# Kernel tuning notes

Measured on AMD Instinct MI355X. Metric: run time of the kernel, lower is better.

Reference implementation:

```python
import jax, jax.numpy as jnp
import numpy as np

IMG = 128; P = 16; ND = IMG // P; N = ND * ND  # 64 patches
INF = 3 * P * P      # 768 flattened patch features
ATT = 768; HID = 3072; OUT = 768; B = 64
EPS = 1e-5


def setup_inputs() -> dict:
    key = jax.random.key(0)
    ks = jax.random.split(key, 24)
    w = lambda k, shape: jax.random.normal(k, shape, jnp.float32) * 0.02
    return {
        "x": jax.random.normal(ks[0], (B, 3, IMG, IMG), jnp.float32),
        # per-patch q/k/v projections: [n, in, out] weights, [n, out] biases
        "Wq": w(ks[1], (N, INF, ATT)), "bq": w(ks[2], (N, ATT)),
        "Wk": w(ks[3], (N, INF, ATT)), "bk": w(ks[4], (N, ATT)),
        "Wv": w(ks[5], (N, INF, ATT)), "bv": w(ks[6], (N, ATT)),
        "ln_g": jnp.ones((ATT,), jnp.float32), "ln_b": jnp.zeros((ATT,), jnp.float32),
        "p1_w": w(ks[7], (INF, ATT)), "p1_b": w(ks[8], (ATT,)),
        "w0": w(ks[9], (ATT, HID)),  "b0": w(ks[10], (HID,)),
        "w1": w(ks[11], (HID, HID)), "b1": w(ks[12], (HID,)),
        "w2": w(ks[13], (HID, HID)), "b2": w(ks[14], (HID,)),
        "w3": w(ks[15], (HID, HID)), "b3": w(ks[16], (HID,)),
        "w4": w(ks[17], (HID, OUT)), "b4": w(ks[18], (OUT,)),
        "p2_w": w(ks[19], (ATT, OUT)), "p2_b": w(ks[20], (OUT,)),
    }


def _forward(x, Wq, bq, Wk, bk, Wv, bv, ln_g, ln_b, p1_w, p1_b,
             w0, b0, w1, b1, w2, b2, w3, b3, w4, b4, p2_w, p2_b):
    b_ = x.shape[0]
    # patch split (row-major over (i,j) blocks) then flatten channel*patch dims
    flat = x.reshape(b_, 3, ND, P, ND, P).transpose(0, 2, 4, 1, 3, 5).reshape(b_, N, INF)
    # per-patch projections, attention taken ACROSS the batch dim (as in source)
    q = jnp.einsum('bnf,nfd->bnd', flat, Wq) + bq
    k = jnp.einsum('bnf,nfd->bnd', flat, Wk) + bk
    v = jnp.einsum('bnf,nfd->bnd', flat, Wv) + bv
    scores = jnp.einsum('bnd,cnd->nbc', q, k) / jnp.sqrt(jnp.float32(ATT))  # [n,B,B]
    attn = jnp.einsum('nbc,cnd->bnd', jax.nn.softmax(scores, axis=-1), v)  # [B,n,ATT]
    # LayerNorm(att_features)
    mu = attn.mean(-1, keepdims=True)
    var = ((attn - mu) ** 2).mean(-1, keepdims=True)
    ln = (attn - mu) / jnp.sqrt(var + EPS) * ln_g + ln_b
    att = ln + flat @ p1_w + p1_b
    # linear stack (no nonlinearity in the source)
    h = att @ w0 + b0
    h = h @ w1 + b1
    h = h @ w2 + b2
    h = h @ w3 + b3
    h = h @ w4 + b4
    proj = h + att @ p2_w + p2_b
    return jax.nn.softmax(proj, axis=2)


def reference(x, Wq, bq, Wk, bk, Wv, bv, ln_g, ln_b, p1_w, p1_b,
              w0, b0, w1, b1, w2, b2, w3, b3, w4, b4, p2_w, p2_b):
    return _forward(x, Wq, bq, Wk, bk, Wv, bv, ln_g, ln_b, p1_w, p1_b,
                    w0, b0, w1, b1, w2, b2, w3, b3, w4, b4, p2_w, p2_b)
```

## Files before the change

kernel.cpp:

```cpp
#include <hip/hip_runtime.h>
#include <hip/hip_bf16.h>

using bf16 = __bf16;
using bf16x8 = __bf16 __attribute__((ext_vector_type(8)));
using f32x4 = float __attribute__((ext_vector_type(4)));

static constexpr long ROWEL = 64L * 768;

__device__ __forceinline__ void async16(void* lds, const void* g)
{
    __builtin_amdgcn_global_load_lds((const __attribute__((address_space(1))) void*)g,
                                     (__attribute__((address_space(3))) void*)lds, 16, 0, 0);
}

__global__ __launch_bounds__(256) void k_patchify(const float* __restrict__ x, bf16* __restrict__ flat)
{
    const int n = blockIdx.x;
    const int b = blockIdx.y;
    const int i_ = n >> 3, j_ = n & 7;
    for (int it = 0; it < 3; ++it) {
        int f = threadIdx.x + it * 256;
        int c = f >> 8, rem = f & 255, pi = rem >> 4, pj = rem & 15;
        float v = x[(((long)(b * 3 + c)) << 14) + ((i_ * 16 + pi) << 7) + (j_ * 16 + pj)];
        flat[(long)b * ROWEL + n * 768 + f] = (bf16)v;
    }
}

__global__ __launch_bounds__(256) void k_cvt_t(const float* __restrict__ W, bf16* __restrict__ Wt,
                                               int Kd, int Nd)
{
    __shared__ bf16 T[64 * 66];
    const int k0 = blockIdx.x * 64, n0 = blockIdx.y * 64;
    const int tid = threadIdx.x;
    const int kr = tid >> 4, nc = (tid & 15) * 4;
#pragma unroll
    for (int i = 0; i < 4; ++i) {
        f32x4 v = *(const f32x4*)(W + (long)(k0 + kr + i * 16) * Nd + n0 + nc);
#pragma unroll
        for (int e = 0; e < 4; ++e)
            T[(kr + i * 16) * 66 + nc + e] = (bf16)v[e];
    }
    __syncthreads();
    const int nr = tid >> 3, ks = (tid & 7) * 8;
#pragma unroll
    for (int it = 0; it < 2; ++it) {
        int n = nr + it * 32;
        bf16x8 o;
#pragma unroll
        for (int j = 0; j < 8; ++j) o[j] = T[(ks + j) * 66 + n];
        *(bf16x8*)(Wt + (long)(n0 + n) * Kd + k0 + ks) = o;
    }
}

__global__ __launch_bounds__(256) void k_cast(const float* __restrict__ W, bf16* __restrict__ o, long nelem)
{
    long i = ((long)blockIdx.x * 256 + threadIdx.x) * 8;
    if (i >= nelem) return;
    f32x4 a = *(const f32x4*)(W + i);
    f32x4 b = *(const f32x4*)(W + i + 4);
    bf16x8 v;
#pragma unroll
    for (int e = 0; e < 4; ++e) { v[e] = (bf16)a[e]; v[4 + e] = (bf16)b[e]; }
    *(bf16x8*)(o + i) = v;
}

template<int BM, int BN>
__global__ __launch_bounds__(256) void k_gemm_bt(
    const bf16* __restrict__ A, long lda,
    const bf16* __restrict__ Bt, long ldb,
    int K,
    const float* __restrict__ bias,
    const float* __restrict__ addm,
    bf16* __restrict__ Cb, float* __restrict__ Cf, long ldc)
{
    constexpr int WM = BM / 2, WN = BN / 2, FM = WM / 16, FN = WN / 16;
    __shared__ bf16 As[BM * 32];
    __shared__ bf16 Bs[BN * 32];
    const int tid = threadIdx.x, lane = tid & 63, wave = tid >> 6;
    const int wm = wave >> 1, wn = wave & 1;
    const long m0 = (long)blockIdx.x * BM, n0 = (long)blockIdx.y * BN;

    f32x4 acc[FM][FN];
#pragma unroll
    for (int i = 0; i < FM; ++i)
#pragma unroll
        for (int j = 0; j < FN; ++j) acc[i][j] = (f32x4){0.f, 0.f, 0.f, 0.f};

    const int nk = K >> 5;
    for (int kt = 0; kt < nk; ++kt) {
        const long kb = (long)kt * 32;
#pragma unroll
        for (int i = 0; i < BM / 64; ++i) {
            const int idx = tid + i * 256;
            const int r = idx >> 2, seg = idx & 3;
            async16(&As[(i * 256 + wave * 64) * 8], A + (m0 + r) * lda + kb + seg * 8);
        }
#pragma unroll
        for (int i = 0; i < BN / 64; ++i) {
            const int idx = tid + i * 256;
            const int r = idx >> 2, seg = idx & 3;
            async16(&Bs[(i * 256 + wave * 64) * 8], Bt + (n0 + r) * ldb + kb + seg * 8);
        }
        __syncthreads();
        bf16x8 af[FM], bfr[FN];
#pragma unroll
        for (int i = 0; i < FM; ++i)
            af[i] = *(const bf16x8*)&As[(wm * WM + i * 16 + (lane & 15)) * 32 + (lane >> 4) * 8];
#pragma unroll
        for (int j = 0; j < FN; ++j)
            bfr[j] = *(const bf16x8*)&Bs[(wn * WN + j * 16 + (lane & 15)) * 32 + (lane >> 4) * 8];
#pragma unroll
        for (int i = 0; i < FM; ++i)
#pragma unroll
            for (int j = 0; j < FN; ++j)
                acc[i][j] = __builtin_amdgcn_mfma_f32_16x16x32_bf16(af[i], bfr[j], acc[i][j], 0, 0, 0);
        __syncthreads();
    }

#pragma unroll
    for (int j = 0; j < FN; ++j) {
        const long col = n0 + wn * WN + j * 16 + (lane & 15);
        const float bb = bias ? bias[col] : 0.f;
#pragma unroll
        for (int i = 0; i < FM; ++i) {
#pragma unroll
            for (int r = 0; r < 4; ++r) {
                const long row = m0 + wm * WM + i * 16 + (lane >> 4) * 4 + r;
                const long idx = row * ldc + col;
                float v = acc[i][j][r] + bb;
                if (addm) v += addm[idx];
                if (Cb) Cb[idx] = (bf16)v;
                if (Cf) Cf[idx] = v;
            }
        }
    }
}

__global__ __launch_bounds__(256) void k_qkv(
    const bf16* __restrict__ flat, const float* __restrict__ W, const float* __restrict__ bias,
    bf16* __restrict__ out)
{
    __shared__ bf16 As[64 * 32];
    __shared__ float Bs[32 * 64];
    const int tid = threadIdx.x, lane = tid & 63, wave = tid >> 6;
    const int wm = wave >> 1, wn = wave & 1;
    const int n0 = blockIdx.x * 64;
    const int z = blockIdx.y;
    const float* Wz = W + (long)z * 589824;

    f32x4 acc[2][2];
#pragma unroll
    for (int i = 0; i < 2; ++i)
#pragma unroll
        for (int j = 0; j < 2; ++j) acc[i][j] = (f32x4){0.f, 0.f, 0.f, 0.f};

    for (int kt = 0; kt < 24; ++kt) {
        const int kb = kt * 32;
        {
            const int r = tid >> 2, seg = tid & 3;
            async16(&As[wave * 512], flat + (long)r * ROWEL + z * 768 + kb + seg * 8);
        }
#pragma unroll
        for (int i = 0; i < 2; ++i) {
            const int g = i * 4 + wave;
            const int kk = kb + g * 4 + (lane >> 4);
            const int nn = (lane & 15) * 4;
            async16(&Bs[g * 256], Wz + (long)kk * 768 + n0 + nn);
        }
        __syncthreads();
        bf16x8 af[2], bfr[2];
#pragma unroll
        for (int i = 0; i < 2; ++i)
            af[i] = *(const bf16x8*)&As[(wm * 32 + i * 16 + (lane & 15)) * 32 + (lane >> 4) * 8];
#pragma unroll
        for (int j = 0; j < 2; ++j) {
            const int n = wn * 32 + j * 16 + (lane & 15);
            const int kf = (lane >> 4) * 8;
            bf16x8 b;
#pragma unroll
            for (int e = 0; e < 8; ++e) b[e] = (bf16)Bs[(kf + e) * 64 + n];
            bfr[j] = b;
        }
#pragma unroll
        for (int i = 0; i < 2; ++i)
#pragma unroll
            for (int j = 0; j < 2; ++j)
                acc[i][j] = __builtin_amdgcn_mfma_f32_16x16x32_bf16(af[i], bfr[j], acc[i][j], 0, 0, 0);
        __syncthreads();
    }

#pragma unroll
    for (int j = 0; j < 2; ++j) {
        const int col = n0 + wn * 32 + j * 16 + (lane & 15);
        const float bb = bias[z * 768 + col];
#pragma unroll
        for (int i = 0; i < 2; ++i) {
#pragma unroll
            for (int r = 0; r < 4; ++r) {
                const int row = wm * 32 + i * 16 + (lane >> 4) * 4 + r;
                out[(long)row * ROWEL + z * 768 + col] = (bf16)(acc[i][j][r] + bb);
            }
        }
    }
}

__global__ __launch_bounds__(256) void k_vm(
    const float* __restrict__ vin, const float* __restrict__ W,
    int K, int N, float* __restrict__ outP)
{
    __shared__ float red[4][64];
    const int tid = threadIdx.x;
    const int nl = tid & 63, kq = tid >> 6;
    const int n = blockIdx.x * 64 + nl;
    const int kc = blockIdx.y;
    const int kchunk = K / 8, kslice = kchunk / 4;
    const int k0 = kc * kchunk + kq * kslice;
    float acc = 0.f;
#pragma unroll 8
    for (int k = k0; k < k0 + kslice; ++k)
        acc += vin[k] * W[(long)k * N + n];
    red[kq][nl] = acc;
    __syncthreads();
    if (kq == 0)
        outP[(long)kc * N + n] = red[0][nl] + red[1][nl] + red[2][nl] + red[3][nl];
}

__global__ __launch_bounds__(256) void k_vred(
    const float* __restrict__ P, const float* __restrict__ b1, const float* __restrict__ b2,
    int N, float* __restrict__ out)
{
    const int n = blockIdx.x * 256 + threadIdx.x;
    if (n >= N) return;
    float s = b1[n] + (b2 ? b2[n] : 0.f);
#pragma unroll
    for (int j = 0; j < 8; ++j) s += P[(long)j * N + n];
    out[n] = s;
}

__global__ __launch_bounds__(256) void k_madd(const float* __restrict__ MTf, const float* __restrict__ p2w,
                                              bf16* __restrict__ Mt)
{
    const int n = blockIdx.x;
    for (int k = threadIdx.x; k < 768; k += 256)
        Mt[n * 768 + k] = (bf16)(MTf[n * 768 + k] + p2w[(long)k * 768 + n]);
}

__global__ __launch_bounds__(256) void k_attn(
    const bf16* __restrict__ q, const bf16* __restrict__ k, const bf16* __restrict__ v,
    float* __restrict__ attn)
{
    const int n = blockIdx.x;
    __shared__ bf16 QT[64 * 72];
    __shared__ bf16 KT[64 * 72];
    __shared__ float S[64 * 66];
    __shared__ bf16 P[64 * 72];
    __shared__ bf16 VT[128 * 72];

    const int tid = threadIdx.x, lane = tid & 63, wave = tid >> 6;
    const int wm = wave >> 1, wn = wave & 1;

    f32x4 accs[2][2];
#pragma unroll
    for (int i = 0; i < 2; ++i)
#pragma unroll
        for (int j = 0; j < 2; ++j) accs[i][j] = (f32x4){0.f, 0.f, 0.f, 0.f};

    for (int kt = 0; kt < 12; ++kt) {
#pragma unroll
        for (int i = 0; i < 2; ++i) {
            int cid = tid + i * 256;
            int r = cid >> 3, seg = cid & 7;
            *(bf16x8*)&QT[r * 72 + seg * 8] = *(const bf16x8*)(q + (long)r * ROWEL + n * 768 + kt * 64 + seg * 8);
            *(bf16x8*)&KT[r * 72 + seg * 8] = *(const bf16x8*)(k + (long)r * ROWEL + n * 768 + kt * 64 + seg * 8);
        }
        __syncthreads();
#pragma unroll
        for (int ks = 0; ks < 2; ++ks) {
            bf16x8 qa[2], kb[2];
#pragma unroll
            for (int i = 0; i < 2; ++i)
                qa[i] = *(const bf16x8*)&QT[(wm * 32 + i * 16 + (lane & 15)) * 72 + ks * 32 + (lane >> 4) * 8];
#pragma unroll
            for (int j = 0; j < 2; ++j)
                kb[j] = *(const bf16x8*)&KT[(wn * 32 + j * 16 + (lane & 15)) * 72 + ks * 32 + (lane >> 4) * 8];
#pragma unroll
            for (int i = 0; i < 2; ++i)
#pragma unroll
                for (int j = 0; j < 2; ++j)
                    accs[i][j] = __builtin_amdgcn_mfma_f32_16x16x32_bf16(qa[i], kb[j], accs[i][j], 0, 0, 0);
        }
        __syncthreads();
    }
    const float sc = 0.03608439182435161f;
#pragma unroll
    for (int i = 0; i < 2; ++i)
#pragma unroll
        for (int j = 0; j < 2; ++j)
#pragma unroll
            for (int r = 0; r < 4; ++r)
                S[(wm * 32 + i * 16 + (lane >> 4) * 4 + r) * 66 + wn * 32 + j * 16 + (lane & 15)] = accs[i][j][r] * sc;
    __syncthreads();

    {
        int r = tid >> 2, l4 = tid & 3;
        float m = -1e30f;
        for (int c = l4; c < 64; c += 4) m = fmaxf(m, S[r * 66 + c]);
        m = fmaxf(m, __shfl_xor(m, 1));
        m = fmaxf(m, __shfl_xor(m, 2));
        float s = 0.f;
        for (int c = l4; c < 64; c += 4) { float e = __expf(S[r * 66 + c] - m); S[r * 66 + c] = e; s += e; }
        s += __shfl_xor(s, 1);
        s += __shfl_xor(s, 2);
        float inv = 1.f / s;
        for (int c = l4; c < 64; c += 4) P[r * 72 + c] = (bf16)(S[r * 66 + c] * inv);
    }
    __syncthreads();

    for (int dc = 0; dc < 6; ++dc) {
#pragma unroll
        for (int i = 0; i < 4; ++i) {
            int cid = tid + i * 256;
            int c = cid >> 4, seg = cid & 15;
            bf16x8 vv = *(const bf16x8*)(v + (long)c * ROWEL + n * 768 + dc * 128 + seg * 8);
#pragma unroll
            for (int e = 0; e < 8; ++e)
                VT[(seg * 8 + e) * 72 + c] = vv[e];
        }
        __syncthreads();
        f32x4 acco[2][4];
#pragma unroll
        for (int i = 0; i < 2; ++i)
#pragma unroll
            for (int j = 0; j < 4; ++j) acco[i][j] = (f32x4){0.f, 0.f, 0.f, 0.f};
#pragma unroll
        for (int ks = 0; ks < 2; ++ks) {
            bf16x8 pa[2], vb[4];
#pragma unroll
            for (int i = 0; i < 2; ++i)
                pa[i] = *(const bf16x8*)&P[(wm * 32 + i * 16 + (lane & 15)) * 72 + ks * 32 + (lane >> 4) * 8];
#pragma unroll
            for (int j = 0; j < 4; ++j)
                vb[j] = *(const bf16x8*)&VT[(wn * 64 + j * 16 + (lane & 15)) * 72 + ks * 32 + (lane >> 4) * 8];
#pragma unroll
            for (int i = 0; i < 2; ++i)
#pragma unroll
                for (int j = 0; j < 4; ++j)
                    acco[i][j] = __builtin_amdgcn_mfma_f32_16x16x32_bf16(pa[i], vb[j], acco[i][j], 0, 0, 0);
        }
#pragma unroll
        for (int i = 0; i < 2; ++i)
#pragma unroll
            for (int j = 0; j < 4; ++j)
#pragma unroll
                for (int r = 0; r < 4; ++r) {
                    long b = wm * 32 + i * 16 + (lane >> 4) * 4 + r;
                    int d = dc * 128 + wn * 64 + j * 16 + (lane & 15);
                    attn[b * ROWEL + n * 768 + d] = acco[i][j][r];
                }
        __syncthreads();
    }
}

__global__ __launch_bounds__(256) void k_ln(float* __restrict__ a,
                                            const float* __restrict__ g, const float* __restrict__ bb)
{
    const long row = blockIdx.x * 4 + (threadIdx.x >> 6);
    const int lane = threadIdx.x & 63;
    float* p = a + row * 768;
    f32x4 xv[3];
    float s = 0.f;
#pragma unroll
    for (int c = 0; c < 3; ++c) {
        xv[c] = *(const f32x4*)(p + c * 256 + lane * 4);
        s += xv[c][0] + xv[c][1] + xv[c][2] + xv[c][3];
    }
#pragma unroll
    for (int o = 1; o < 64; o <<= 1) s += __shfl_xor(s, o);
    const float mu = s * (1.f / 768.f);
    float vs = 0.f;
#pragma unroll
    for (int c = 0; c < 3; ++c)
#pragma unroll
        for (int e = 0; e < 4; ++e) { float d = xv[c][e] - mu; vs += d * d; }
#pragma unroll
    for (int o = 1; o < 64; o <<= 1) vs += __shfl_xor(vs, o);
    const float rstd = rsqrtf(vs * (1.f / 768.f) + 1e-5f);
#pragma unroll
    for (int c = 0; c < 3; ++c)
#pragma unroll
        for (int e = 0; e < 4; ++e) {
            int col = c * 256 + lane * 4 + e;
            p[col] = (xv[c][e] - mu) * rstd * g[col] + bb[col];
        }
}

__global__ __launch_bounds__(256) void k_softmax(float* __restrict__ o)
{
    const long row = blockIdx.x * 4 + (threadIdx.x >> 6);
    const int lane = threadIdx.x & 63;
    float* p = o + row * 768;
    f32x4 xv[3];
    float m = -1e30f;
#pragma unroll
    for (int c = 0; c < 3; ++c) {
        xv[c] = *(const f32x4*)(p + c * 256 + lane * 4);
        m = fmaxf(m, fmaxf(fmaxf(xv[c][0], xv[c][1]), fmaxf(xv[c][2], xv[c][3])));
    }
#pragma unroll
    for (int o2 = 1; o2 < 64; o2 <<= 1) m = fmaxf(m, __shfl_xor(m, o2));
    float s = 0.f;
#pragma unroll
    for (int c = 0; c < 3; ++c)
#pragma unroll
        for (int e = 0; e < 4; ++e) { float ev = __expf(xv[c][e] - m); xv[c][e] = ev; s += ev; }
#pragma unroll
    for (int o2 = 1; o2 < 64; o2 <<= 1) s += __shfl_xor(s, o2);
    const float inv = 1.f / s;
#pragma unroll
    for (int c = 0; c < 3; ++c)
        *(f32x4*)(p + c * 256 + lane * 4) = xv[c] * inv;
}

extern "C" void kernel_launch(void* const* d_in, const int* in_sizes, int n_in,
                              void* d_out, int out_size, void* d_ws, size_t ws_size,
                              hipStream_t stream)
{
    const float* x   = (const float*)d_in[0];
    const float* Wq  = (const float*)d_in[1];
    const float* bq  = (const float*)d_in[2];
    const float* Wk  = (const float*)d_in[3];
    const float* bk  = (const float*)d_in[4];
    const float* Wv  = (const float*)d_in[5];
    const float* bv  = (const float*)d_in[6];
    const float* lng = (const float*)d_in[7];
    const float* lnb = (const float*)d_in[8];
    const float* p1w = (const float*)d_in[9];
    const float* p1b = (const float*)d_in[10];
    const float* w0  = (const float*)d_in[11];
    const float* b0  = (const float*)d_in[12];
    const float* w1  = (const float*)d_in[13];
    const float* b1  = (const float*)d_in[14];
    const float* w2  = (const float*)d_in[15];
    const float* b2  = (const float*)d_in[16];
    const float* w3  = (const float*)d_in[17];
    const float* b3  = (const float*)d_in[18];
    const float* w4  = (const float*)d_in[19];
    const float* b4  = (const float*)d_in[20];
    const float* p2w = (const float*)d_in[21];
    const float* p2b = (const float*)d_in[22];
    float* out = (float*)d_out;

    char* wsbase = (char*)d_ws;
    size_t off = 0;
    auto alloc = [&](size_t bytes) { char* p = wsbase + off; off += (bytes + 255) & ~(size_t)255; return p; };
    bf16*  flat = (bf16*)alloc(4096L * 768 * 2);
    bf16*  qb   = (bf16*)alloc(4096L * 768 * 2);
    bf16*  kb   = (bf16*)alloc(4096L * 768 * 2);
    bf16*  vb2  = (bf16*)alloc(4096L * 768 * 2);
    float* attn = (float*)alloc(4096L * 768 * 4);
    bf16*  att  = (bf16*)alloc(4096L * 768 * 2);
    bf16*  p1t  = (bf16*)alloc(768L * 768 * 2);
    bf16*  w0c  = (bf16*)alloc(768L * 3072 * 2);
    bf16*  w1c  = (bf16*)alloc(3072L * 3072 * 2);
    bf16*  w2c  = (bf16*)alloc(3072L * 3072 * 2);
    bf16*  w3c  = (bf16*)alloc(3072L * 3072 * 2);
    bf16*  w4t  = (bf16*)alloc(768L * 3072 * 2);
    bf16*  M1   = (bf16*)alloc(768L * 3072 * 2);
    bf16*  M2   = (bf16*)alloc(768L * 3072 * 2);
    float* MTf  = (float*)alloc(768L * 768 * 4);
    bf16*  Mt   = (bf16*)alloc(768L * 768 * 2);
    float* vP   = (float*)alloc(8L * 3072 * 4);
    float* c1   = (float*)alloc(3072 * 4);
    float* c2   = (float*)alloc(3072 * 4);
    float* c3   = (float*)alloc(3072 * 4);
    float* c4   = (float*)alloc(768 * 4);
    if (off > ws_size) return;

    k_patchify<<<dim3(64, 64), 256, 0, stream>>>(x, flat);
    k_qkv<<<dim3(12, 64), 256, 0, stream>>>(flat, Wq, bq, qb);
    k_qkv<<<dim3(12, 64), 256, 0, stream>>>(flat, Wk, bk, kb);
    k_qkv<<<dim3(12, 64), 256, 0, stream>>>(flat, Wv, bv, vb2);
    k_attn<<<64, 256, 0, stream>>>(qb, kb, vb2, attn);
    k_ln<<<1024, 256, 0, stream>>>(attn, lng, lnb);
    k_cvt_t<<<dim3(12, 12), 256, 0, stream>>>(p1w, p1t, 768, 768);
    k_gemm_bt<64, 128><<<dim3(64, 6), 256, 0, stream>>>(flat, 768, p1t, 768, 768, p1b, attn, att, nullptr, 768);

    k_cvt_t<<<dim3(48, 12), 256, 0, stream>>>(w4, w4t, 3072, 768);
    k_cast<<<4608, 256, 0, stream>>>(w1, w1c, 3072L * 3072);
    k_cast<<<4608, 256, 0, stream>>>(w2, w2c, 3072L * 3072);
    k_cast<<<4608, 256, 0, stream>>>(w3, w3c, 3072L * 3072);
    k_cast<<<1152, 256, 0, stream>>>(w0, w0c, 768L * 3072);

    k_gemm_bt<64, 128><<<dim3(12, 24), 256, 0, stream>>>(w4t, 3072, w3c, 3072, 3072, nullptr, nullptr, M1, nullptr, 3072);
    k_gemm_bt<64, 128><<<dim3(12, 24), 256, 0, stream>>>(M1, 3072, w2c, 3072, 3072, nullptr, nullptr, M2, nullptr, 3072);
    k_gemm_bt<64, 128><<<dim3(12, 24), 256, 0, stream>>>(M2, 3072, w1c, 3072, 3072, nullptr, nullptr, M1, nullptr, 3072);
    k_gemm_bt<64, 64><<<dim3(12, 12), 256, 0, stream>>>(M1, 3072, w0c, 3072, 3072, nullptr, nullptr, nullptr, MTf, 768);
    k_madd<<<768, 256, 0, stream>>>(MTf, p2w, Mt);

    k_vm<<<dim3(48, 8), 256, 0, stream>>>(b0, w1, 3072, 3072, vP);
    k_vred<<<12, 256, 0, stream>>>(vP, b1, nullptr, 3072, c1);
    k_vm<<<dim3(48, 8), 256, 0, stream>>>(c1, w2, 3072, 3072, vP);
    k_vred<<<12, 256, 0, stream>>>(vP, b2, nullptr, 3072, c2);
    k_vm<<<dim3(48, 8), 256, 0, stream>>>(c2, w3, 3072, 3072, vP);
    k_vred<<<12, 256, 0, stream>>>(vP, b3, nullptr, 3072, c3);
    k_vm<<<dim3(12, 8), 256, 0, stream>>>(c3, w4, 3072, 768, vP);
    k_vred<<<3, 256, 0, stream>>>(vP, b4, p2b, 768, c4);

    k_gemm_bt<64, 128><<<dim3(64, 6), 256, 0, stream>>>(att, 768, Mt, 768, 768, c4, nullptr, nullptr, out, 768);
    k_softmax<<<1024, 256, 0, stream>>>(out);
}
```

Baseline: 509.9 us.

## Double-buffer GEMM staging, batch launches, fuse bias-chain reductions and transpose-add epilogue

Adds double-buffered LDS staging to the generic GEMM and the per-patch QKV kernel so the next K tile loads while the current one computes. Merges the QKV, cast and transpose launches into single grids using blockIdx.z or y, folds the p2_w transposed add into the last weight-chain GEMM epilogue (removing k_madd and the fp32 intermediate), and fuses the bias-chain partial reductions into the next vector-matrix kernel reading bf16 weights. The weight-chain GEMMs switch to 64x64 tiles for more blocks. Reading bf16 weights in the bias chain lowers precision slightly, and the transposed add in the epilogue reads with a strided pattern.

Result: slower. 606.5 us (+19.0%).

```diff
diff --git a/kernel.cpp b/kernel.cpp
--- a/kernel.cpp
+++ b/kernel.cpp
@@ -26,9 +26,15 @@
     }
 }
 
-__global__ __launch_bounds__(256) void k_cvt_t(const float* __restrict__ W, bf16* __restrict__ Wt,
-                                               int Kd, int Nd)
-{
+__global__ __launch_bounds__(256) void k_cvt_t2(
+    const float* __restrict__ W0, bf16* __restrict__ T0,
+    const float* __restrict__ W1, bf16* __restrict__ T1)
+{
+    const int z = blockIdx.z;
+    const float* W = z ? W1 : W0;
+    bf16* Wt = z ? T1 : T0;
+    const int Kd = z ? 768 : 3072, Nd = 768;
+    if (z && blockIdx.x >= 12) return;
     __shared__ bf16 T[64 * 66];
     const int k0 = blockIdx.x * 64, n0 = blockIdx.y * 64;
     const int tid = threadIdx.x;
@@ -52,8 +58,16 @@
     }
 }
 
-__global__ __launch_bounds__(256) void k_cast(const float* __restrict__ W, bf16* __restrict__ o, long nelem)
-{
+__global__ __launch_bounds__(256) void k_cast4(
+    const float* __restrict__ s0, bf16* __restrict__ d0,
+    const float* __restrict__ s1, bf16* __restrict__ d1,
+    const float* __restrict__ s2, bf16* __restrict__ d2,
+    const float* __restrict__ s3, bf16* __restrict__ d3)
+{
+    const int z = blockIdx.y;
+    const float* W = z == 0 ? s0 : z == 1 ? s1 : z == 2 ? s2 : s3;
+    bf16* o = z == 0 ? d0 : z == 1 ? d1 : z == 2 ? d2 : d3;
+    const long nelem = z == 0 ? 768L * 3072 : 3072L * 3072;
     long i = ((long)blockIdx.x * 256 + threadIdx.x) * 8;
     if (i >= nelem) return;
     f32x4 a = *(const f32x4*)(W + i);
@@ -71,11 +85,12 @@
     int K,
     const float* __restrict__ bias,
     const float* __restrict__ addm,
+    const float* __restrict__ addt, long atld,
     bf16* __restrict__ Cb, float* __restrict__ Cf, long ldc)
 {
     constexpr int WM = BM / 2, WN = BN / 2, FM = WM / 16, FN = WN / 16;
-    __shared__ bf16 As[BM * 32];
-    __shared__ bf16 Bs[BN * 32];
+    __shared__ bf16 As[2][BM * 32];
+    __shared__ bf16 Bs[2][BN * 32];
     const int tid = threadIdx.x, lane = tid & 63, wave = tid >> 6;
     const int wm = wave >> 1, wn = wave & 1;
     const long m0 = (long)blockIdx.x * BM, n0 = (long)blockIdx.y * BN;
@@ -87,34 +102,42 @@
         for (int j = 0; j < FN; ++j) acc[i][j] = (f32x4){0.f, 0.f, 0.f, 0.f};
 
     const int nk = K >> 5;
+
+    auto stage = [&](int buf, int kt) {
+        const long kb = (long)kt * 32;
+#pragma unroll
+        for (int i = 0; i < BM / 64; ++i) {
+            const int c = i * 256 + tid;
+            const int r = c >> 2, seg = c & 3;
+            async16(&As[buf][(i * 256 + wave * 64) * 8], A + (m0 + r) * lda + kb + seg * 8);
+        }
+#pragma unroll
+        for (int i = 0; i < BN / 64; ++i) {
+            const int c = i * 256 + tid;
+            const int r = c >> 2, seg = c & 3;
+            async16(&Bs[buf][(i * 256 + wave * 64) * 8], Bt + (n0 + r) * ldb + kb + seg * 8);
+        }
+    };
+
+    stage(0, 0);
+    __syncthreads();
+    int cur = 0;
     for (int kt = 0; kt < nk; ++kt) {
-        const long kb = (long)kt * 32;
-#pragma unroll
-        for (int i = 0; i < BM / 64; ++i) {
-            const int idx = tid + i * 256;
-            const int r = idx >> 2, seg = idx & 3;
-            async16(&As[(i * 256 + wave * 64) * 8], A + (m0 + r) * lda + kb + seg * 8);
-        }
-#pragma unroll
-        for (int i = 0; i < BN / 64; ++i) {
-            const int idx = tid + i * 256;
-            const int r = idx >> 2, seg = idx & 3;
-            async16(&Bs[(i * 256 + wave * 64) * 8], Bt + (n0 + r) * ldb + kb + seg * 8);
-        }
-        __syncthreads();
+        if (kt + 1 < nk) stage(cur ^ 1, kt + 1);
         bf16x8 af[FM], bfr[FN];
 #pragma unroll
         for (int i = 0; i < FM; ++i)
-            af[i] = *(const bf16x8*)&As[(wm * WM + i * 16 + (lane & 15)) * 32 + (lane >> 4) * 8];
+            af[i] = *(const bf16x8*)&As[cur][(wm * WM + i * 16 + (lane & 15)) * 32 + (lane >> 4) * 8];
 #pragma unroll
         for (int j = 0; j < FN; ++j)
-            bfr[j] = *(const bf16x8*)&Bs[(wn * WN + j * 16 + (lane & 15)) * 32 + (lane >> 4) * 8];
+            bfr[j] = *(const bf16x8*)&Bs[cur][(wn * WN + j * 16 + (lane & 15)) * 32 + (lane >> 4) * 8];
 #pragma unroll
         for (int i = 0; i < FM; ++i)
 #pragma unroll
             for (int j = 0; j < FN; ++j)
                 acc[i][j] = __builtin_amdgcn_mfma_f32_16x16x32_bf16(af[i], bfr[j], acc[i][j], 0, 0, 0);
         __syncthreads();
+        cur ^= 1;
     }
 
 #pragma unroll
@@ -129,6 +152,7 @@
                 const long idx = row * ldc + col;
                 float v = acc[i][j][r] + bb;
                 if (addm) v += addm[idx];
+                if (addt) v += addt[col * atld + row];
                 if (Cb) Cb[idx] = (bf16)v;
                 if (Cf) Cf[idx] = v;
             }
@@ -137,11 +161,18 @@
 }
 
 __global__ __launch_bounds__(256) void k_qkv(
-    const bf16* __restrict__ flat, const float* __restrict__ W, const float* __restrict__ bias,
-    bf16* __restrict__ out)
-{
-    __shared__ bf16 As[64 * 32];
-    __shared__ float Bs[32 * 64];
+    const bf16* __restrict__ flat,
+    const float* __restrict__ Wq, const float* __restrict__ Wk, const float* __restrict__ Wv,
+    const float* __restrict__ bq, const float* __restrict__ bk, const float* __restrict__ bv,
+    bf16* __restrict__ qo, bf16* __restrict__ ko, bf16* __restrict__ vo)
+{
+    const int zz = blockIdx.z;
+    const float* W = zz == 0 ? Wq : zz == 1 ? Wk : Wv;
+    const float* bias = zz == 0 ? bq : zz == 1 ? bk : bv;
+    bf16* out = zz == 0 ? qo : zz == 1 ? ko : vo;
+
+    __shared__ bf16 As[2][64 * 32];
+    __shared__ float Bs[2][32 * 64];
     const int tid = threadIdx.x, lane = tid & 63, wave = tid >> 6;
     const int wm = wave >> 1, wn = wave & 1;
     const int n0 = blockIdx.x * 64;
@@ -154,31 +185,36 @@
 #pragma unroll
         for (int j = 0; j < 2; ++j) acc[i][j] = (f32x4){0.f, 0.f, 0.f, 0.f};
 
-    for (int kt = 0; kt < 24; ++kt) {
+    auto stage = [&](int buf, int kt) {
         const int kb = kt * 32;
         {
             const int r = tid >> 2, seg = tid & 3;
-            async16(&As[wave * 512], flat + (long)r * ROWEL + z * 768 + kb + seg * 8);
+            async16(&As[buf][wave * 512], flat + (long)r * ROWEL + z * 768 + kb + seg * 8);
         }
 #pragma unroll
         for (int i = 0; i < 2; ++i) {
-            const int g = i * 4 + wave;
-            const int kk = kb + g * 4 + (lane >> 4);
-            const int nn = (lane & 15) * 4;
-            async16(&Bs[g * 256], Wz + (long)kk * 768 + n0 + nn);
-        }
-        __syncthreads();
+            const int c = i * 256 + tid;
+            const int kl = c >> 4, nn = (c & 15) * 4;
+            async16(&Bs[buf][(i * 256 + wave * 64) * 4], Wz + (long)(kb + kl) * 768 + n0 + nn);
+        }
+    };
+
+    stage(0, 0);
+    __syncthreads();
+    int cur = 0;
+    for (int kt = 0; kt < 24; ++kt) {
+        if (kt + 1 < 24) stage(cur ^ 1, kt + 1);
         bf16x8 af[2], bfr[2];
 #pragma unroll
         for (int i = 0; i < 2; ++i)
-            af[i] = *(const bf16x8*)&As[(wm * 32 + i * 16 + (lane & 15)) * 32 + (lane >> 4) * 8];
+            af[i] = *(const bf16x8*)&As[cur][(wm * 32 + i * 16 + (lane & 15)) * 32 + (lane >> 4) * 8];
 #pragma unroll
         for (int j = 0; j < 2; ++j) {
             const int n = wn * 32 + j * 16 + (lane & 15);
             const int kf = (lane >> 4) * 8;
             bf16x8 b;
 #pragma unroll
-            for (int e = 0; e < 8; ++e) b[e] = (bf16)Bs[(kf + e) * 64 + n];
+            for (int e = 0; e < 8; ++e) b[e] = (bf16)Bs[cur][(kf + e) * 64 + n];
             bfr[j] = b;
         }
 #pragma unroll
@@ -187,6 +223,7 @@
             for (int j = 0; j < 2; ++j)
                 acc[i][j] = __builtin_amdgcn_mfma_f32_16x16x32_bf16(af[i], bfr[j], acc[i][j], 0, 0, 0);
         __syncthreads();
+        cur ^= 1;
     }
 
 #pragma unroll
@@ -204,9 +241,10 @@
     }
 }
 
-__global__ __launch_bounds__(256) void k_vm(
-    const float* __restrict__ vin, const float* __restrict__ W,
-    int K, int N, float* __restrict__ outP)
+template<typename TW>
+__global__ __launch_bounds__(256) void k_vm2(
+    const float* __restrict__ Pin, const float* __restrict__ bin, const TW* __restrict__ W,
+    int K, int N, float* __restrict__ Pout)
 {
     __shared__ float red[4][64];
     const int tid = threadIdx.x;
@@ -216,13 +254,19 @@
     const int kchunk = K / 8, kslice = kchunk / 4;
     const int k0 = kc * kchunk + kq * kslice;
     float acc = 0.f;
-#pragma unroll 8
-    for (int k = k0; k < k0 + kslice; ++k)
-        acc += vin[k] * W[(long)k * N + n];
+#pragma unroll 4
+    for (int k = k0; k < k0 + kslice; ++k) {
+        float vk = bin[k];
+        if (Pin) {
+#pragma unroll
+            for (int j = 0; j < 8; ++j) vk += Pin[(long)j * K + k];
+        }
+        acc += vk * (float)W[(long)k * N + n];
+    }
     red[kq][nl] = acc;
     __syncthreads();
     if (kq == 0)
-        outP[(long)kc * N + n] = red[0][nl] + red[1][nl] + red[2][nl] + red[3][nl];
+        Pout[(long)kc * N + n] = red[0][nl] + red[1][nl] + red[2][nl] + red[3][nl];
 }
 
 __global__ __launch_bounds__(256) void k_vred(
@@ -235,14 +279,6 @@
 #pragma unroll
     for (int j = 0; j < 8; ++j) s += P[(long)j * N + n];
     out[n] = s;
-}
-
-__global__ __launch_bounds__(256) void k_madd(const float* __restrict__ MTf, const float* __restrict__ p2w,
-                                              bf16* __restrict__ Mt)
-{
-    const int n = blockIdx.x;
-    for (int k = threadIdx.x; k < 768; k += 256)
-        Mt[n * 768 + k] = (bf16)(MTf[n * 768 + k] + p2w[(long)k * 768 + n]);
 }
 
 __global__ __launch_bounds__(256) void k_attn(
@@ -460,52 +496,41 @@
     float* attn = (float*)alloc(4096L * 768 * 4);
     bf16*  att  = (bf16*)alloc(4096L * 768 * 2);
     bf16*  p1t  = (bf16*)alloc(768L * 768 * 2);
+    bf16*  w4t  = (bf16*)alloc(768L * 3072 * 2);
     bf16*  w0c  = (bf16*)alloc(768L * 3072 * 2);
     bf16*  w1c  = (bf16*)alloc(3072L * 3072 * 2);
     bf16*  w2c  = (bf16*)alloc(3072L * 3072 * 2);
     bf16*  w3c  = (bf16*)alloc(3072L * 3072 * 2);
-    bf16*  w4t  = (bf16*)alloc(768L * 3072 * 2);
     bf16*  M1   = (bf16*)alloc(768L * 3072 * 2);
     bf16*  M2   = (bf16*)alloc(768L * 3072 * 2);
-    float* MTf  = (float*)alloc(768L * 768 * 4);
+    bf16*  M3   = (bf16*)alloc(768L * 3072 * 2);
     bf16*  Mt   = (bf16*)alloc(768L * 768 * 2);
-    float* vP   = (float*)alloc(8L * 3072 * 4);
-    float* c1   = (float*)alloc(3072 * 4);
-    float* c2   = (float*)alloc(3072 * 4);
-    float* c3   = (float*)alloc(3072 * 4);
+    float* vPa  = (float*)alloc(8L * 3072 * 4);
+    float* vPb  = (float*)alloc(8L * 3072 * 4);
     float* c4   = (float*)alloc(768 * 4);
     if (off > ws_size) return;
 
     k_patchify<<<dim3(64, 64), 256, 0, stream>>>(x, flat);
-    k_qkv<<<dim3(12, 64), 256, 0, stream>>>(flat, Wq, bq, qb);
-    k_qkv<<<dim3(12, 64), 256, 0, stream>>>(flat, Wk, bk, kb);
-    k_qkv<<<dim3(12, 64), 256, 0, stream>>>(flat, Wv, bv, vb2);
+    k_cast4<<<dim3(4608, 4), 256, 0, stream>>>(w0, w0c, w1, w1c, w2, w2c, w3, w3c);
+    k_cvt_t2<<<dim3(48, 12, 2), 256, 0, stream>>>(w4, w4t, p1w, p1t);
+
+    k_qkv<<<dim3(12, 64, 3), 256, 0, stream>>>(flat, Wq, Wk, Wv, bq, bk, bv, qb, kb, vb2);
+
     k_attn<<<64, 256, 0, stream>>>(qb, kb, vb2, attn);
     k_ln<<<1024, 256, 0, stream>>>(attn, lng, lnb);
-    k_cvt_t<<<dim3(12, 12), 256, 0, stream>>>(p1w, p1t, 768, 768);
-    k_gemm_bt<64, 128><<<dim3(64, 6), 256, 0, stream>>>(flat, 768, p1t, 768, 768, p1b, attn, att, nullptr, 768);
-
-    k_cvt_t<<<dim3(48, 12), 256, 0, stream>>>(w4, w4t, 3072, 768);
-    k_cast<<<4608, 256, 0, stream>>>(w1, w1c, 3072L * 3072);
-    k_cast<<<4608, 256, 0, stream>>>(w2, w2c, 3072L * 3072);
-    k_cast<<<4608, 256, 0, stream>>>(w3, w3c, 3072L * 3072);
-    k_cast<<<1152, 256, 0, stream>>>(w0, w0c, 768L * 3072);
-
-    k_gemm_bt<64, 128><<<dim3(12, 24), 256, 0, stream>>>(w4t, 3072, w3c, 3072, 3072, nullptr, nullptr, M1, nullptr, 3072);
-    k_gemm_bt<64, 128><<<dim3(12, 24), 256, 0, stream>>>(M1, 3072, w2c, 3072, 3072, nullptr, nullptr, M2, nullptr, 3072);
-    k_gemm_bt<64, 128><<<dim3(12, 24), 256, 0, stream>>>(M2, 3072, w1c, 3072, 3072, nullptr, nullptr, M1, nullptr, 3072);
-    k_gemm_bt<64, 64><<<dim3(12, 12), 256, 0, stream>>>(M1, 3072, w0c, 3072, 3072, nullptr, nullptr, nullptr, MTf, 768);
-    k_madd<<<768, 256, 0, stream>>>(MTf, p2w, Mt);
-
-    k_vm<<<dim3(48, 8), 256, 0, stream>>>(b0, w1, 3072, 3072, vP);
-    k_vred<<<12, 256, 0, stream>>>(vP, b1, nullptr, 3072, c1);
-    k_vm<<<dim3(48, 8), 256, 0, stream>>>(c1, w2, 3072, 3072, vP);
-    k_vred<<<12, 256, 0, stream>>>(vP, b2, nullptr, 3072, c2);
-    k_vm<<<dim3(48, 8), 256, 0, stream>>>(c2, w3, 3072, 3072, vP);
-    k_vred<<<12, 256, 0, stream>>>(vP, b3, nullptr, 3072, c3);
-    k_vm<<<dim3(12, 8), 256, 0, stream>>>(c3, w4, 3072, 768, vP);
-    k_vred<<<3, 256, 0, stream>>>(vP, b4, p2b, 768, c4);
-
-    k_gemm_bt<64, 128><<<dim3(64, 6), 256, 0, stream>>>(att, 768, Mt, 768, 768, c4, nullptr, nullptr, out, 768);
+    k_gemm_bt<64, 128><<<dim3(64, 6), 256, 0, stream>>>(flat, 768, p1t, 768, 768, p1b, attn, nullptr, 0, att, nullptr, 768);
+
+    k_gemm_bt<64, 64><<<dim3(12, 48), 256, 0, stream>>>(w4t, 3072, w3c, 3072, 3072, nullptr, nullptr, nullptr, 0, M1, nullptr, 3072);
+    k_gemm_bt<64, 64><<<dim3(12, 48), 256, 0, stream>>>(M1, 3072, w2c, 3072, 3072, nullptr, nullptr, nullptr, 0, M2, nullptr, 3072);
+    k_gemm_bt<64, 64><<<dim3(12, 48), 256, 0, stream>>>(M2, 3072, w1c, 3072, 3072, nullptr, nullptr, nullptr, 0, M3, nullptr, 3072);
+    k_gemm_bt<64, 64><<<dim3(12, 12), 256, 0, stream>>>(M3, 3072, w0c, 3072, 3072, nullptr, nullptr, p2w, 768, Mt, nullptr, 768);
+
+    k_vm2<bf16><<<dim3(48, 8), 256, 0, stream>>>(nullptr, b0, w1c, 3072, 3072, vPa);
+    k_vm2<bf16><<<dim3(48, 8), 256, 0, stream>>>(vPa, b1, w2c, 3072, 3072, vPb);
+    k_vm2<bf16><<<dim3(48, 8), 256, 0, stream>>>(vPb, b2, w3c, 3072, 3072, vPa);
+    k_vm2<float><<<dim3(12, 8), 256, 0, stream>>>(vPa, b3, w4, 3072, 768, vPb);
+    k_vred<<<3, 256, 0, stream>>>(vPb, b4, p2b, 768, c4);
+
+    k_gemm_bt<64, 128><<<dim3(64, 6), 256, 0, stream>>>(att, 768, Mt, 768, 768, c4, nullptr, nullptr, 0, nullptr, out, 768);
     k_softmax<<<1024, 256, 0, stream>>>(out);
 }
```
